# Performance work log

Hardware: AMD Instinct MI355X
Metric: run time of the kernel (lower is better)

Reference implementation:

```python
import jax, jax.numpy as jnp
import numpy as np
from jax import lax

V_VOX, T_PTS, D, H, W = 12000, 35, 10, 200, 176
EPS = 1e-5


def _bn(x, g, b, axes, shape):
    m = x.mean(axes, keepdims=True)
    v = x.var(axes, keepdims=True)  # biased var, matches torch BN training stats
    return g.reshape(shape) * (x - m) * lax.rsqrt(v + EPS) + b.reshape(shape)


def _conv3d(x, w, b):
    y = lax.conv_general_dilated(x, w, (1, 1, 1), 'SAME',
                                 dimension_numbers=('NCDHW', 'OIDHW', 'NCDHW'))
    return y + b[None, :, None, None, None]


def _conv2d(x, w, b):
    y = lax.conv_general_dilated(x, w, (1, 1), 'SAME',
                                 dimension_numbers=('NCHW', 'OIHW', 'NCHW'))
    return y + b[None, :, None, None]


def setup_inputs() -> dict:
    key = jax.random.key(0)
    ks = jax.random.split(key, 12)
    voxels = jax.random.normal(ks[0], (1, V_VOX, T_PTS, 4), jnp.float32)
    # unique voxel coordinates (the torch loop overwrites on duplicates; unique avoids ambiguity)
    rng = np.random.default_rng(0)
    flat = rng.choice(D * H * W, size=V_VOX, replace=False)
    z = flat // (H * W); rem = flat % (H * W)
    coords = jnp.asarray(np.stack([z, rem // W, rem % W], axis=1), dtype=jnp.int32)
    s = 0.05
    p = dict(
        w_lin=jax.random.normal(ks[1], (32, 4), jnp.float32) * s,
        b_lin=jnp.zeros((32,), jnp.float32),
        g_bn0=jnp.ones((32,), jnp.float32), be_bn0=jnp.zeros((32,), jnp.float32),
        w_c3a=jax.random.normal(ks[2], (64, 32, 3, 3, 3), jnp.float32) * s,
        b_c3a=jnp.zeros((64,), jnp.float32),
        g_bn1=jnp.ones((64,), jnp.float32), be_bn1=jnp.zeros((64,), jnp.float32),
        w_c3b=jax.random.normal(ks[3], (64, 64, 3, 3, 3), jnp.float32) * s,
        b_c3b=jnp.zeros((64,), jnp.float32),
        g_bn2=jnp.ones((64,), jnp.float32), be_bn2=jnp.zeros((64,), jnp.float32),
        w_r1=jax.random.normal(ks[4], (128, 64, 3, 3), jnp.float32) * s,
        b_r1=jnp.zeros((128,), jnp.float32),
        w_r2=jax.random.normal(ks[5], (8, 128, 1, 1), jnp.float32) * s,
        b_r2=jnp.zeros((8,), jnp.float32),
    )
    return dict(voxels=voxels, coords=coords, **p)


def reference(voxels, coords, w_lin, b_lin, g_bn0, be_bn0,
              w_c3a, b_c3a, g_bn1, be_bn1, w_c3b, b_c3b, g_bn2, be_bn2,
              w_r1, b_r1, w_r2, b_r2):
    B, V, T, C = voxels.shape
    # SimpleVFE: linear -> BN1d (batch stats) -> relu -> max over points
    h = voxels.reshape(B * V * T, C) @ w_lin.T + b_lin          # [BVT,32]
    h = jax.nn.relu(_bn(h, g_bn0, be_bn0, 0, (1, 32)))
    feats = h.reshape(B, V, T, 32).max(axis=2)                  # [B,V,32]
    # fused scatter into dense volume (replaces per-voxel python loop)
    volume = jnp.zeros((B, 32, D, H, W), voxels.dtype)
    volume = volume.at[0, :, coords[:, 0], coords[:, 1], coords[:, 2]].set(feats[0])
    # 3D backbone
    x = jax.nn.relu(_bn(_conv3d(volume, w_c3a, b_c3a), g_bn1, be_bn1, (0, 2, 3, 4), (1, 64, 1, 1, 1)))
    x = jax.nn.relu(_bn(_conv3d(x, w_c3b, b_c3b), g_bn2, be_bn2, (0, 2, 3, 4), (1, 64, 1, 1, 1)))
    x = x.mean(axis=2)                                          # collapse depth -> [B,64,H,W]
    # RPN head
    out = _conv2d(jax.nn.relu(_conv2d(x, w_r1, b_r1)), w_r2, b_r2)  # [B,8,H,W]
    box = jnp.concatenate([out[:, 0:3], jnp.exp(out[:, 3:6]),
                           jnp.tanh(out[:, 6:7]), jax.nn.sigmoid(out[:, 7:8])], axis=1)
    return box
```

## Files before the change

kernel.cpp:

```cpp
#include <hip/hip_runtime.h>
#include <math.h>

#define V_VOX 12000
#define T_PTS 35
#define DD 10
#define HH 200
#define WW 176
#define EPSV 1e-5f

#define DP 12
#define HP 202
#define WP 178
#define PPLN (HP * WP)
#define PVOX (DP * PPLN)
#define NPIX (DD * HH * WW)
#define HWPIX (HH * WW)

typedef _Float16 half_t;
typedef _Float16 f16x8 __attribute__((ext_vector_type(8)));
typedef float f32x4 __attribute__((ext_vector_type(4)));

#define WPA_OFF 0
#define WPB_OFF 110592
#define WPR1_OFF 331776
#define STATS_OFF 479232
#define FEATS_OFF 483328
#define VOLP_OFF 2019328
#define X1P_OFF 29633536
#define Y_OFF 84861952
#define PLANE_OFF 129917952
#define R1OUT_OFF 134520320

#define S_BN0S 0
#define S_BN0Q 32
#define S_BN1S 64
#define S_BN1Q 128
#define S_BN2S 192
#define S_BN2Q 256
#define C0A 320
#define C0B 352
#define C1A 384
#define C1B 448
#define C2A 512
#define C2B 576

#define CLDS 40

__global__ void k_pack(const float* __restrict__ w, half_t* __restrict__ wp,
                       int IC, int NT, int OC) {
    int id = blockIdx.x * 256 + threadIdx.x;
    int OCT = OC >> 4, KH = IC >> 5;
    int total = NT * KH * OCT * 512;
    if (id >= total) return;
    int j = id & 7;
    int lane = (id >> 3) & 63;
    int rest = id >> 9;
    int ot = rest % OCT; rest /= OCT;
    int kh = rest % KH;
    int tap = rest / KH;
    int oc = ot * 16 + (lane & 15);
    int ic = kh * 32 + (lane >> 4) * 8 + j;
    wp[id] = (half_t)w[(oc * IC + ic) * NT + tap];
}

__global__ void k_vfe_stats(const float4* __restrict__ vox, const float* __restrict__ w_lin,
                            const float* __restrict__ b_lin, float* __restrict__ S) {
    int tid = blockIdx.x * 256 + threadIdx.x;
    int c = threadIdx.x & 31;
    float4 w = ((const float4*)w_lin)[c];
    float bl = b_lin[c];
    float s = 0.f, q = 0.f;
    const int np = V_VOX * T_PTS;
    int stride = gridDim.x * 8;
    for (int p = tid >> 5; p < np; p += stride) {
        float4 v = vox[p];
        float d = v.x * w.x + v.y * w.y + v.z * w.z + v.w * w.w + bl;
        s += d;
        q += d * d;
    }
    s += __shfl_xor(s, 32);
    q += __shfl_xor(q, 32);
    if ((threadIdx.x & 63) < 32) {
        atomicAdd(&S[S_BN0S + c], s);
        atomicAdd(&S[S_BN0Q + c], q);
    }
}

__global__ void k_bn_final(const float* __restrict__ ss, const float* __restrict__ sq,
                           const float* __restrict__ g, const float* __restrict__ be,
                           float* __restrict__ ca, float* __restrict__ cb, int C, float invN) {
    int c = threadIdx.x;
    if (c >= C) return;
    float m = ss[c] * invN;
    float v = sq[c] * invN - m * m;
    float a = g[c] * rsqrtf(v + EPSV);
    ca[c] = a;
    cb[c] = be[c] - m * a;
}

__global__ void k_vfe_max(const float4* __restrict__ vox, const float* __restrict__ w_lin,
                          const float* __restrict__ b_lin, const float* __restrict__ ca,
                          const float* __restrict__ cb, float* __restrict__ feats) {
    int id = blockIdx.x * 256 + threadIdx.x;
    if (id >= V_VOX * 32) return;
    int c = id & 31;
    int v = id >> 5;
    float4 w = ((const float4*)w_lin)[c];
    float bl = b_lin[c], A = ca[c], B = cb[c];
    float m = 0.f;
    for (int t = 0; t < T_PTS; t++) {
        float4 p = vox[v * T_PTS + t];
        float d = p.x * w.x + p.y * w.y + p.z * w.z + p.w * w.w + bl;
        m = fmaxf(m, A * d + B);
    }
    feats[id] = m;
}

__global__ void k_scatter(const float* __restrict__ feats, const int* __restrict__ coords,
                          half_t* __restrict__ volp) {
    int id = blockIdx.x * 256 + threadIdx.x;
    if (id >= V_VOX * 32) return;
    int c = id & 31;
    int v = id >> 5;
    int z = coords[v * 3 + 0];
    int y = coords[v * 3 + 1];
    int x = coords[v * 3 + 2];
    volp[(((z + 1) * HP + (y + 1)) * WP + (x + 1)) * 32 + c] = (half_t)feats[id];
}

template <int KH, int DZ, int OCTP, bool RELU, bool STATS>
__global__ __launch_bounds__(256, 2) void k_conv(const half_t* __restrict__ in,
                                                 size_t khstride,
                                                 const half_t* __restrict__ wp,
                                                 const float* __restrict__ bias,
                                                 half_t* __restrict__ out,
                                                 float* __restrict__ ssum,
                                                 float* __restrict__ ssq) {
    constexpr int OC = OCTP * 16;
    constexpr int TOT8 = 18 * 18 * 4;
    constexpr int NS = DZ * KH;
    __shared__ half_t tA[18 * 18 * CLDS];
    __shared__ half_t tB[9 * 4 * 512];

    const int tid = threadIdx.x;
    const int lane = tid & 63;
    const int wv = tid >> 6;
    const int x0 = blockIdx.x * 16;
    const int y0b = blockIdx.y * 16;
    const int z0 = (DZ == 3) ? blockIdx.z : 0;
    const int ocb = (DZ == 3) ? 0 : blockIdx.z * 4;
    const int y0w = y0b + wv * 4;
    const bool valid = (y0w < HH);
    const int colc = lane & 15, grp = lane >> 4;

    f32x4 acc[4][4];
#pragma unroll
    for (int m = 0; m < 4; m++)
#pragma unroll
        for (int n = 0; n < 4; n++) acc[m][n] = (f32x4)(0.f);

#pragma unroll 1
    for (int s = 0; s < NS; ++s) {
        const int dz = s / KH, kh = s % KH;
        const half_t* sl = in + (size_t)kh * khstride
                           + (size_t)(z0 + dz) * (DZ == 3 ? (size_t)PPLN * 32 : 0);
#pragma unroll
        for (int it = 0; it < 6; ++it) {
            int e = it * 256 + tid;
            if (e < TOT8) {
                int ch8 = e & 3;
                int pxr = e >> 2;
                int px = pxr % 18;
                int row = pxr / 18;
                int srow = y0b + row;
                if (srow > HP - 1) srow = HP - 1;
                *(f16x8*)&tA[pxr * CLDS + ch8 * 8] =
                    *(const f16x8*)(sl + ((size_t)srow * WP + x0 + px) * 32 + ch8 * 8);
            }
        }
        const half_t* wb0 = wp + ((size_t)(dz * 9) * KH + kh) * OCTP * 512;
#pragma unroll
        for (int it = 0; it < 9; ++it) {
            int e = it * 256 + tid;
            int c64 = e & 63;
            int unit = e >> 6;
            int ot = unit & 3;
            int tap = unit >> 2;
            *(f16x8*)&tB[unit * 512 + c64 * 8] =
                *(const f16x8*)(wb0 + ((size_t)tap * KH * OCTP + ocb + ot) * 512 + c64 * 8);
        }
        __syncthreads();

        if (valid) {
#pragma unroll
            for (int dx = 0; dx < 3; ++dx) {
                f16x8 Af[6];
#pragma unroll
                for (int r = 0; r < 6; ++r)
                    Af[r] = *(const f16x8*)&tA[((wv * 4 + r) * 18 + colc + dx) * CLDS + grp * 8];
#pragma unroll
                for (int dy = 0; dy < 3; ++dy) {
                    f16x8 Bf[4];
#pragma unroll
                    for (int n = 0; n < 4; ++n)
                        Bf[n] = *(const f16x8*)&tB[((dy * 3 + dx) * 4 + n) * 512 + lane * 8];
#pragma unroll
                    for (int m = 0; m < 4; ++m)
#pragma unroll
                        for (int n = 0; n < 4; ++n)
                            acc[m][n] = __builtin_amdgcn_mfma_f32_16x16x32_f16(
                                Af[dy + m], Bf[n], acc[m][n], 0, 0, 0);
                }
            }
        }
        __syncthreads();
    }

    if (!valid) return;
#pragma unroll
    for (int n = 0; n < 4; ++n) {
        int oc = (ocb + n) * 16 + colc;
        float bv = bias[oc];
        float s = 0.f, q = 0.f;
#pragma unroll
        for (int m = 0; m < 4; ++m) {
            int yy = y0w + m;
#pragma unroll
            for (int i = 0; i < 4; ++i) {
                int xx = x0 + grp * 4 + i;
                float v = acc[m][n][i] + bv;
                if (STATS) { s += v; q += v * v; }
                float w = RELU ? fmaxf(v, 0.f) : v;
                out[((size_t)(z0 * HH + yy) * WW + xx) * OC + oc] = (half_t)w;
            }
        }
        if (STATS) {
            s += __shfl_xor(s, 16); s += __shfl_xor(s, 32);
            q += __shfl_xor(q, 16); q += __shfl_xor(q, 32);
            if (lane < 16) {
                atomicAdd(&ssum[oc], s);
                atomicAdd(&ssq[oc], q);
            }
        }
    }
}

__global__ void k_activate(const half_t* __restrict__ y1, const float* __restrict__ ca,
                           const float* __restrict__ cb, half_t* __restrict__ xp) {
    int id = blockIdx.x * 256 + threadIdx.x;
    if (id >= PVOX * 8) return;
    int c0 = (id & 7) * 8;
    int pix = id >> 3;
    int zp = pix / PPLN;
    int rem = pix - zp * PPLN;
    int yp = rem / WP;
    int xq = rem - yp * WP;
    f16x8 o;
    if (zp >= 1 && zp <= DD && yp >= 1 && yp <= HH && xq >= 1 && xq <= WW) {
        size_t p = ((size_t)((zp - 1) * HH + (yp - 1)) * WW + (xq - 1));
        f16x8 v = *(const f16x8*)(y1 + p * 64 + c0);
#pragma unroll
        for (int j = 0; j < 8; j++)
            o[j] = (half_t)fmaxf(ca[c0 + j] * (float)v[j] + cb[c0 + j], 0.f);
    } else {
#pragma unroll
        for (int j = 0; j < 8; j++) o[j] = (half_t)0.f;
    }
    int khp = c0 >> 5;
    *(f16x8*)(xp + (size_t)khp * PVOX * 32 + (size_t)pix * 32 + (c0 & 31)) = o;
}

__global__ void k_depthmean(const half_t* __restrict__ y2, const float* __restrict__ ca,
                            const float* __restrict__ cb, half_t* __restrict__ plane) {
    int id = blockIdx.x * 256 + threadIdx.x;
    int c = id & 63;
    int pix = id >> 6;
    int yp = pix / WP;
    int xq = pix - yp * WP;
    float val = 0.f;
    if (yp >= 1 && yp <= HH && xq >= 1 && xq <= WW) {
        float A = ca[c], B = cb[c], s = 0.f;
        const half_t* base = y2 + ((size_t)(yp - 1) * WW + (xq - 1)) * 64 + c;
#pragma unroll
        for (int z = 0; z < DD; z++)
            s += fmaxf(A * (float)base[(size_t)z * HWPIX * 64] + B, 0.f);
        val = s * 0.1f;
    }
    int khp = c >> 5;
    plane[(size_t)khp * PPLN * 32 + (size_t)pix * 32 + (c & 31)] = (half_t)val;
}

__global__ void k_r2(const half_t* __restrict__ r1o, const float* __restrict__ w,
                     const float* __restrict__ bias, float* __restrict__ outp) {
    __shared__ float wsm[1024];
    for (int i = threadIdx.x; i < 1024; i += 256) wsm[i] = w[i];
    __syncthreads();
    int p = blockIdx.x * 256 + threadIdx.x;
    if (p >= HWPIX) return;
    float acc[8];
#pragma unroll
    for (int o = 0; o < 8; o++) acc[o] = bias[o];
    const half_t* rb = r1o + (size_t)p * 128;
#pragma unroll 4
    for (int icb = 0; icb < 128; icb += 8) {
        f16x8 v = *(const f16x8*)(rb + icb);
#pragma unroll
        for (int j = 0; j < 8; j++) {
            float vv = (float)v[j];
#pragma unroll
            for (int o = 0; o < 8; o++) acc[o] += vv * wsm[o * 128 + icb + j];
        }
    }
    outp[0 * HWPIX + p] = acc[0];
    outp[1 * HWPIX + p] = acc[1];
    outp[2 * HWPIX + p] = acc[2];
    outp[3 * HWPIX + p] = expf(acc[3]);
    outp[4 * HWPIX + p] = expf(acc[4]);
    outp[5 * HWPIX + p] = expf(acc[5]);
    outp[6 * HWPIX + p] = tanhf(acc[6]);
    outp[7 * HWPIX + p] = 1.f / (1.f + expf(-acc[7]));
}

extern "C" void kernel_launch(void* const* d_in, const int* in_sizes, int n_in,
                              void* d_out, int out_size, void* d_ws, size_t ws_size,
                              hipStream_t stream) {
    const float4* voxels = (const float4*)d_in[0];
    const int* coords = (const int*)d_in[1];
    const float* w_lin = (const float*)d_in[2];
    const float* b_lin = (const float*)d_in[3];
    const float* g_bn0 = (const float*)d_in[4];
    const float* be_bn0 = (const float*)d_in[5];
    const float* w_c3a = (const float*)d_in[6];
    const float* b_c3a = (const float*)d_in[7];
    const float* g_bn1 = (const float*)d_in[8];
    const float* be_bn1 = (const float*)d_in[9];
    const float* w_c3b = (const float*)d_in[10];
    const float* b_c3b = (const float*)d_in[11];
    const float* g_bn2 = (const float*)d_in[12];
    const float* be_bn2 = (const float*)d_in[13];
    const float* w_r1 = (const float*)d_in[14];
    const float* b_r1 = (const float*)d_in[15];
    const float* w_r2 = (const float*)d_in[16];
    const float* b_r2 = (const float*)d_in[17];

    char* ws = (char*)d_ws;
    half_t* wpA = (half_t*)(ws + WPA_OFF);
    half_t* wpB = (half_t*)(ws + WPB_OFF);
    half_t* wpR1 = (half_t*)(ws + WPR1_OFF);
    float* S = (float*)(ws + STATS_OFF);
    float* feats = (float*)(ws + FEATS_OFF);
    half_t* volp = (half_t*)(ws + VOLP_OFF);
    half_t* x1p = (half_t*)(ws + X1P_OFF);
    half_t* Y = (half_t*)(ws + Y_OFF);
    half_t* plane = (half_t*)(ws + PLANE_OFF);
    half_t* r1out = (half_t*)(ws + R1OUT_OFF);
    float* outp = (float*)d_out;

    hipMemsetAsync(S, 0, 320 * sizeof(float), stream);
    hipMemsetAsync(volp, 0, (size_t)PVOX * 32 * sizeof(half_t), stream);

    k_pack<<<216, 256, 0, stream>>>(w_c3a, wpA, 32, 27, 64);
    k_pack<<<432, 256, 0, stream>>>(w_c3b, wpB, 64, 27, 64);
    k_pack<<<288, 256, 0, stream>>>(w_r1, wpR1, 64, 9, 128);

    k_vfe_stats<<<512, 256, 0, stream>>>(voxels, w_lin, b_lin, S);
    k_bn_final<<<1, 64, 0, stream>>>(S + S_BN0S, S + S_BN0Q, g_bn0, be_bn0,
                                     S + C0A, S + C0B, 32, 1.f / 420000.f);
    k_vfe_max<<<1500, 256, 0, stream>>>(voxels, w_lin, b_lin, S + C0A, S + C0B, feats);
    k_scatter<<<1500, 256, 0, stream>>>(feats, coords, volp);

    k_conv<1, 3, 4, false, true><<<dim3(11, 13, 10), 256, 0, stream>>>(
        volp, 0, wpA, b_c3a, Y, S + S_BN1S, S + S_BN1Q);
    k_bn_final<<<1, 64, 0, stream>>>(S + S_BN1S, S + S_BN1Q, g_bn1, be_bn1,
                                     S + C1A, S + C1B, 64, 1.f / 352000.f);
    k_activate<<<13484, 256, 0, stream>>>(Y, S + C1A, S + C1B, x1p);

    k_conv<2, 3, 4, false, true><<<dim3(11, 13, 10), 256, 0, stream>>>(
        x1p, (size_t)PVOX * 32, wpB, b_c3b, Y, S + S_BN2S, S + S_BN2Q);
    k_bn_final<<<1, 64, 0, stream>>>(S + S_BN2S, S + S_BN2Q, g_bn2, be_bn2,
                                     S + C2A, S + C2B, 64, 1.f / 352000.f);

    k_depthmean<<<8989, 256, 0, stream>>>(Y, S + C2A, S + C2B, plane);

    k_conv<2, 1, 8, true, false><<<dim3(11, 13, 2), 256, 0, stream>>>(
        plane, (size_t)PPLN * 32, wpR1, b_r1, r1out, nullptr, nullptr);
    k_r2<<<138, 256, 0, stream>>>(r1out, w_r2, b_r2, outp);
}
```

Measured before the change: 490.8 us.

## Use direct global-to-LDS loads with swizzled layout and split output channels in conv

The conv kernel now stages input and weight tiles with global_load_lds (16-byte direct-to-LDS copies), so data no longer passes through registers. The input tile uses an XOR-swizzled layout instead of padding to avoid LDS bank conflicts. Each block now computes 32 output channels instead of 64, which doubles the grid, halves the accumulators and raises launch bounds to 4 blocks per CU for more occupancy. In exchange, input tiles are loaded twice across the channel halves, and the loop now waits on vmcnt(0) with no overlap between loads and compute.

After: 456.2 us. 7.1% less time.

```diff
diff --git a/kernel.cpp b/kernel.cpp
--- a/kernel.cpp
+++ b/kernel.cpp
@@ -44,7 +44,11 @@
 #define C2A 512
 #define C2B 576
 
-#define CLDS 40
+__device__ __forceinline__ void gload16(const half_t* g, half_t* l) {
+    __builtin_amdgcn_global_load_lds(
+        (const __attribute__((address_space(1))) void*)g,
+        (__attribute__((address_space(3))) void*)l, 16, 0, 0);
+}
 
 __global__ void k_pack(const float* __restrict__ w, half_t* __restrict__ wp,
                        int IC, int NT, int OC) {
@@ -129,7 +133,7 @@
 }
 
 template <int KH, int DZ, int OCTP, bool RELU, bool STATS>
-__global__ __launch_bounds__(256, 2) void k_conv(const half_t* __restrict__ in,
+__global__ __launch_bounds__(256, 4) void k_conv(const half_t* __restrict__ in,
                                                  size_t khstride,
                                                  const half_t* __restrict__ wp,
                                                  const float* __restrict__ bias,
@@ -137,27 +141,43 @@
                                                  float* __restrict__ ssum,
                                                  float* __restrict__ ssq) {
     constexpr int OC = OCTP * 16;
-    constexpr int TOT8 = 18 * 18 * 4;
     constexpr int NS = DZ * KH;
-    __shared__ half_t tA[18 * 18 * CLDS];
-    __shared__ half_t tB[9 * 4 * 512];
+    __shared__ __align__(16) half_t tA[21 * 512];
+    __shared__ __align__(16) half_t tB[18 * 512];
 
     const int tid = threadIdx.x;
     const int lane = tid & 63;
     const int wv = tid >> 6;
     const int x0 = blockIdx.x * 16;
     const int y0b = blockIdx.y * 16;
-    const int z0 = (DZ == 3) ? blockIdx.z : 0;
-    const int ocb = (DZ == 3) ? 0 : blockIdx.z * 4;
+    const int bz = blockIdx.z;
+    const int z0 = (DZ == 3) ? (bz >> 1) : 0;
+    const int ocb = (DZ == 3) ? (bz & 1) * 2 : bz * 2;
     const int y0w = y0b + wv * 4;
     const bool valid = (y0w < HH);
     const int colc = lane & 15, grp = lane >> 4;
 
-    f32x4 acc[4][4];
+    unsigned gofsA[6];
+#pragma unroll
+    for (int i = 0; i < 6; ++i) {
+        int run = wv + 4 * i;
+        int c = run * 64 + lane;
+        if (c > 1295) c = 1295;
+        int pixhi = c >> 3, s = c & 7;
+        int b = ((s >> 2) ^ (pixhi >> 1)) & 1;
+        int q = ((s ^ b) & 1) | ((((s >> 1) ^ pixhi) & 1) << 1);
+        int pix = pixhi * 2 + b;
+        int row = pix / 18, px = pix - row * 18;
+        int srow = y0b + row;
+        if (srow > HP - 1) srow = HP - 1;
+        gofsA[i] = (unsigned)((srow * WP + x0 + px) * 32 + q * 8);
+    }
+
+    f32x4 acc[4][2];
 #pragma unroll
     for (int m = 0; m < 4; m++)
 #pragma unroll
-        for (int n = 0; n < 4; n++) acc[m][n] = (f32x4)(0.f);
+        for (int n = 0; n < 2; n++) acc[m][n] = (f32x4)(0.f);
 
 #pragma unroll 1
     for (int s = 0; s < NS; ++s) {
@@ -165,30 +185,21 @@
         const half_t* sl = in + (size_t)kh * khstride
                            + (size_t)(z0 + dz) * (DZ == 3 ? (size_t)PPLN * 32 : 0);
 #pragma unroll
-        for (int it = 0; it < 6; ++it) {
-            int e = it * 256 + tid;
-            if (e < TOT8) {
-                int ch8 = e & 3;
-                int pxr = e >> 2;
-                int px = pxr % 18;
-                int row = pxr / 18;
-                int srow = y0b + row;
-                if (srow > HP - 1) srow = HP - 1;
-                *(f16x8*)&tA[pxr * CLDS + ch8 * 8] =
-                    *(const f16x8*)(sl + ((size_t)srow * WP + x0 + px) * 32 + ch8 * 8);
+        for (int i = 0; i < 6; ++i) {
+            int run = wv + 4 * i;
+            if (run < 21) gload16(sl + gofsA[i], &tA[run * 512]);
+        }
+#pragma unroll
+        for (int i = 0; i < 5; ++i) {
+            int r = wv + 4 * i;
+            if (r < 18) {
+                int tap = r >> 1, hf = r & 1;
+                const half_t* g = wp + (((size_t)(dz * 9 + tap) * KH + kh) * OCTP + ocb + hf) * 512
+                                  + lane * 8;
+                gload16(g, &tB[r * 512]);
             }
         }
-        const half_t* wb0 = wp + ((size_t)(dz * 9) * KH + kh) * OCTP * 512;
-#pragma unroll
-        for (int it = 0; it < 9; ++it) {
-            int e = it * 256 + tid;
-            int c64 = e & 63;
-            int unit = e >> 6;
-            int ot = unit & 3;
-            int tap = unit >> 2;
-            *(f16x8*)&tB[unit * 512 + c64 * 8] =
-                *(const f16x8*)(wb0 + ((size_t)tap * KH * OCTP + ocb + ot) * 512 + c64 * 8);
-        }
+        asm volatile("s_waitcnt vmcnt(0)" ::: "memory");
         __syncthreads();
 
         if (valid) {
@@ -196,18 +207,21 @@
             for (int dx = 0; dx < 3; ++dx) {
                 f16x8 Af[6];
 #pragma unroll
-                for (int r = 0; r < 6; ++r)
-                    Af[r] = *(const f16x8*)&tA[((wv * 4 + r) * 18 + colc + dx) * CLDS + grp * 8];
+                for (int r = 0; r < 6; ++r) {
+                    int pix = (wv * 4 + r) * 18 + colc + dx;
+                    int ah = ((pix << 5) | (grp << 3)) ^ ((pix & 7) << 3);
+                    Af[r] = *(const f16x8*)&tA[ah];
+                }
 #pragma unroll
                 for (int dy = 0; dy < 3; ++dy) {
-                    f16x8 Bf[4];
-#pragma unroll
-                    for (int n = 0; n < 4; ++n)
-                        Bf[n] = *(const f16x8*)&tB[((dy * 3 + dx) * 4 + n) * 512 + lane * 8];
+                    f16x8 Bf[2];
+#pragma unroll
+                    for (int n = 0; n < 2; ++n)
+                        Bf[n] = *(const f16x8*)&tB[((dy * 3 + dx) * 2 + n) * 512 + lane * 8];
 #pragma unroll
                     for (int m = 0; m < 4; ++m)
 #pragma unroll
-                        for (int n = 0; n < 4; ++n)
+                        for (int n = 0; n < 2; ++n)
                             acc[m][n] = __builtin_amdgcn_mfma_f32_16x16x32_f16(
                                 Af[dy + m], Bf[n], acc[m][n], 0, 0, 0);
                 }
@@ -218,7 +232,7 @@
 
     if (!valid) return;
 #pragma unroll
-    for (int n = 0; n < 4; ++n) {
+    for (int n = 0; n < 2; ++n) {
         int oc = (ocb + n) * 16 + colc;
         float bv = bias[oc];
         float s = 0.f, q = 0.f;
@@ -369,20 +383,20 @@
     k_vfe_max<<<1500, 256, 0, stream>>>(voxels, w_lin, b_lin, S + C0A, S + C0B, feats);
     k_scatter<<<1500, 256, 0, stream>>>(feats, coords, volp);
 
-    k_conv<1, 3, 4, false, true><<<dim3(11, 13, 10), 256, 0, stream>>>(
+    k_conv<1, 3, 4, false, true><<<dim3(11, 13, 20), 256, 0, stream>>>(
         volp, 0, wpA, b_c3a, Y, S + S_BN1S, S + S_BN1Q);
     k_bn_final<<<1, 64, 0, stream>>>(S + S_BN1S, S + S_BN1Q, g_bn1, be_bn1,
                                      S + C1A, S + C1B, 64, 1.f / 352000.f);
     k_activate<<<13484, 256, 0, stream>>>(Y, S + C1A, S + C1B, x1p);
 
-    k_conv<2, 3, 4, false, true><<<dim3(11, 13, 10), 256, 0, stream>>>(
+    k_conv<2, 3, 4, false, true><<<dim3(11, 13, 20), 256, 0, stream>>>(
         x1p, (size_t)PVOX * 32, wpB, b_c3b, Y, S + S_BN2S, S + S_BN2Q);
     k_bn_final<<<1, 64, 0, stream>>>(S + S_BN2S, S + S_BN2Q, g_bn2, be_bn2,
                                      S + C2A, S + C2B, 64, 1.f / 352000.f);
 
     k_depthmean<<<8989, 256, 0, stream>>>(Y, S + C2A, S + C2B, plane);
 
-    k_conv<2, 1, 8, true, false><<<dim3(11, 13, 2), 256, 0, stream>>>(
+    k_conv<2, 1, 8, true, false><<<dim3(11, 13, 4), 256, 0, stream>>>(
         plane, (size_t)PPLN * 32, wpR1, b_r1, r1out, nullptr, nullptr);
     k_r2<<<138, 256, 0, stream>>>(r1out, w_r2, b_r2, outp);
 }
```
